# Kernel optimization log

Hardware: AMD Instinct MI355X
Metric: run time of the kernel (lower is better)

Reference implementation:

```python
import jax, jax.numpy as jnp
import numpy as np


def _conv3x3(x, W, b):
    # NCHW conv, stride 1, padding 1 (hard-coded in the torch module)
    y = jax.lax.conv_general_dilated(
        x, W, window_strides=(1, 1), padding=[(1, 1), (1, 1)],
        dimension_numbers=("NCHW", "OIHW", "NCHW"))
    return y + b[None, :, None, None]


def _grid_sample_bilinear(img, gx, gy):
    # img: [N,H,W]; gx,gy: [N,H,W] normalized coords in [-1,1].
    # Matches torch grid_sample(mode='bilinear', padding_mode='zeros',
    # align_corners=False).
    N, H, W = img.shape
    ix = ((gx + 1.0) * W - 1.0) * 0.5  # unnormalized x coord
    iy = ((gy + 1.0) * H - 1.0) * 0.5  # unnormalized y coord

    x0f = jnp.floor(ix)
    y0f = jnp.floor(iy)
    x0 = x0f.astype(jnp.int32)
    y0 = y0f.astype(jnp.int32)
    x1 = x0 + 1
    y1 = y0 + 1

    # bilinear weights
    wx1 = ix - x0f
    wy1 = iy - y0f
    wx0 = 1.0 - wx1
    wy0 = 1.0 - wy1

    n_idx = jnp.arange(N)[:, None, None]

    def gather(yi, xi):
        valid = (yi >= 0) & (yi < H) & (xi >= 0) & (xi < W)
        yc = jnp.clip(yi, 0, H - 1)
        xc = jnp.clip(xi, 0, W - 1)
        v = img[n_idx, yc, xc]
        return jnp.where(valid, v, 0.0)

    return (gather(y0, x0) * (wy0 * wx0)
            + gather(y0, x1) * (wy0 * wx1)
            + gather(y1, x0) * (wy1 * wx0)
            + gather(y1, x1) * (wy1 * wx1))


def setup_inputs() -> dict:
    key = jax.random.key(0)
    ks = jax.random.split(key, 7)
    B, Cin, Cout, H, W = 16, 64, 64, 128, 128
    fan_in = Cin * 3 * 3
    std = 1.0 / np.sqrt(fan_in)
    x = jax.random.normal(ks[0], (B, Cin, H, W), dtype=jnp.float32)
    Ws = jax.random.normal(ks[1], (Cout, Cin, 3, 3), dtype=jnp.float32) * std
    Wx = jax.random.normal(ks[2], (Cout, Cin, 3, 3), dtype=jnp.float32) * std
    Wy = jax.random.normal(ks[3], (Cout, Cin, 3, 3), dtype=jnp.float32) * std
    bs = jnp.zeros((Cout,), dtype=jnp.float32)
    bx = jnp.zeros((Cout,), dtype=jnp.float32)
    by = jnp.zeros((Cout,), dtype=jnp.float32)
    return {"x": x, "Ws": Ws, "bs": bs, "Wx": Wx, "bx": bx, "Wy": Wy, "by": by}


def reference(x, Ws, bs, Wx, bx, Wy, by):
    score = _conv3x3(x, Ws, bs)            # [B,C,H,W]
    gx = _conv3x3(x, Wx, bx)               # absolute grid x coords
    gy = _conv3x3(x, Wy, by)               # absolute grid y coords
    B, C, H, W = score.shape
    out = _grid_sample_bilinear(score.reshape(B * C, H, W),
                                gx.reshape(B * C, H, W),
                                gy.reshape(B * C, H, W))
    return out.reshape(B, C, H, W)
```

## Files before the change

kernel.cpp:

```cpp
#include <hip/hip_runtime.h>
#include <stdint.h>

typedef unsigned short ushort_t;
typedef short bf16x8 __attribute__((ext_vector_type(8)));
typedef float f32x4 __attribute__((ext_vector_type(4)));
typedef float f32x16 __attribute__((ext_vector_type(16)));
typedef unsigned int uint4v __attribute__((ext_vector_type(4)));

#define HW_ 16384

__device__ __forceinline__ float bf2f(ushort_t u){
  return __uint_as_float(((unsigned)u) << 16);
}
__device__ __forceinline__ ushort_t f2bf(float f){
  unsigned u = __float_as_uint(f);
  u += 0x7fffu + ((u >> 16) & 1u);
  return (ushort_t)(u >> 16);
}
#define MFMA __builtin_amdgcn_mfma_f32_32x32x16_bf16

__global__ __launch_bounds__(256) void k_repack(
    const float* __restrict__ Ws, const float* __restrict__ Wx,
    const float* __restrict__ Wy, ushort_t* __restrict__ Wp){
  int e = blockIdx.x*256 + threadIdx.x;
  if (e >= 6*36*64*8) return;
  int j = e & 7; int lane = (e >> 3) & 63; int tt = e >> 9;
  int ks = tt % 36; int mtg = tt / 36;
  int co = mtg*32 + (lane & 31);
  int tap = ks >> 2;
  int ci = (ks & 3)*16 + ((lane >> 5) & 1)*8 + j;
  const float* src; int c;
  if (co < 64)      { src = Ws; c = co;       }
  else if (co < 128){ src = Wx; c = co - 64;  }
  else              { src = Wy; c = co - 128; }
  float w = src[(c*64 + ci)*9 + tap];
  ushort_t hi = f2bf(w);
  if (mtg < 2){
    Wp[e] = hi;
  } else {
    int eg = e - 2*18432;
    Wp[36864  + eg] = hi;
    Wp[110592 + eg] = f2bf(w - bf2f(hi));
  }
}

__global__ __launch_bounds__(256, 2) void k_conv_all(
    const float* __restrict__ x, const ushort_t* __restrict__ Wp,
    const float* __restrict__ bs, const float* __restrict__ bx,
    const float* __restrict__ by,
    ushort_t* __restrict__ score, unsigned int* __restrict__ coords){
  int bid = blockIdx.x;
  int idx = bid >> 3;
  int b = (bid & 7) + 8*(idx >> 7);
  int rest = idx & 127;
  int h0 = (rest >> 1)*2;
  int wq = (rest & 1)*64;
  int t = threadIdx.x; int lane = t & 63; int wid = t >> 6;
  int n = lane & 31; int kh = lane >> 5;
  __shared__ __align__(16) ushort_t XL[2*16896];

  const float* xb = x + (size_t)b*64*HW_;
  #pragma unroll 3
  for (int it=0; it<9; it++){
    int f = it*256 + t;
    if (f < 2112){
      int r   = f / 528;
      int rem = f - r*528;
      int o   = rem / 66;
      int w1  = rem - o*66;
      int y = h0 + r - 1;
      int w = wq + w1 - 1;
      bf16x8 hv = {0,0,0,0,0,0,0,0}, lv = {0,0,0,0,0,0,0,0};
      if (((unsigned)y < 128u) & ((unsigned)w < 128u)){
        const float* p = xb + (size_t)(o*8)*HW_ + y*128 + w;
        #pragma unroll
        for (int j=0;j<8;j++){
          float fv = p[(size_t)j*HW_];
          ushort_t hi = f2bf(fv);
          hv[j] = (short)hi;
          lv[j] = (short)f2bf(fv - bf2f(hi));
        }
      }
      int addr = (r*66 + w1)*64 + ((o ^ (w1 & 7))<<3);
      *(bf16x8*)&XL[addr]         = hv;
      *(bf16x8*)&XL[16896 + addr] = lv;
    }
  }
  __syncthreads();

  int mh = wid & 1;
  int ph = wid >> 1;

  f32x16 acc_s[2], acc_x[2], acc_y[2];
  #pragma unroll
  for (int reg=0; reg<16; reg++){
    int col = mh*32 + (reg & 3) + 8*(reg >> 2) + 4*kh;
    float vs = bs[col], vx = bx[col], vy = by[col];
    #pragma unroll
    for (int ni=0; ni<2; ni++){
      acc_s[ni][reg] = vs; acc_x[ni][reg] = vx; acc_y[ni][reg] = vy;
    }
  }

  const ushort_t* aSb = Wp + mh*36*512 + lane*8;
  const ushort_t* aXh = Wp + 36864 + mh*36*512 + lane*8;
  const ushort_t* aYh = Wp + 36864 + (2+mh)*36*512 + lane*8;
  #pragma unroll
  for (int tap=0; tap<9; tap++){
    int rb = tap/3; int dw = tap - rb*3 - 1;
    int row = rb + ph;
    #pragma unroll
    for (int q=0; q<4; q++){
      int ks = tap*4 + q;
      bf16x8 s8 = *(const bf16x8*)&aSb[ks*512];
      bf16x8 xh = *(const bf16x8*)&aXh[ks*512];
      bf16x8 xl = *(const bf16x8*)&aXh[73728 + ks*512];
      bf16x8 yh = *(const bf16x8*)&aYh[ks*512];
      bf16x8 yl = *(const bf16x8*)&aYh[73728 + ks*512];
      #pragma unroll
      for (int ni=0; ni<2; ni++){
        int w1 = ni*32 + n + dw + 1;
        int off = (row*66 + w1)*64 + ((((q<<1)+kh) ^ (w1 & 7)) << 3);
        bf16x8 bh = *(const bf16x8*)&XL[off];
        bf16x8 bl = *(const bf16x8*)&XL[16896 + off];
        acc_s[ni] = MFMA(s8, bh, acc_s[ni], 0,0,0);
        acc_x[ni] = MFMA(xh, bh, acc_x[ni], 0,0,0);
        acc_y[ni] = MFMA(yh, bh, acc_y[ni], 0,0,0);
        acc_x[ni] = MFMA(xl, bh, acc_x[ni], 0,0,0);
        acc_y[ni] = MFMA(yl, bh, acc_y[ni], 0,0,0);
        acc_x[ni] = MFMA(xh, bl, acc_x[ni], 0,0,0);
        acc_y[ni] = MFMA(yh, bl, acc_y[ni], 0,0,0);
      }
    }
  }

  int h = h0 + ph;
  #pragma unroll
  for (int ni=0; ni<2; ni++){
    int w = wq + ni*32 + n;
    ushort_t*     sb = score  + (size_t)b*64*HW_ + h*128 + w;
    unsigned int* cb = coords + (size_t)b*64*HW_ + h*128 + w;
    #pragma unroll
    for (int reg=0; reg<16; reg++){
      int col = mh*32 + (reg & 3) + 8*(reg >> 2) + 4*kh;
      sb[(size_t)col*HW_] = f2bf(acc_s[ni][reg]);
      float ix = fminf(fmaxf((acc_x[ni][reg]+1.f)*64.f - 0.5f, -2.f), 129.f);
      float iy = fminf(fmaxf((acc_y[ni][reg]+1.f)*64.f - 0.5f, -2.f), 129.f);
      unsigned ux = (unsigned)rintf((ix+2.f)*480.f);
      unsigned uy = (unsigned)rintf((iy+2.f)*480.f);
      cb[(size_t)col*HW_] = ux | (uy << 16);
    }
  }
}

__global__ __launch_bounds__(256, 4) void k_sample(
    const ushort_t* __restrict__ score, const unsigned int* __restrict__ coords,
    float* __restrict__ out){
  int bid = blockIdx.x;
  int idx = bid >> 3;
  int b  = (bid & 7) + 8*(idx >> 6);
  int co = idx & 63;
  int t = threadIdx.x;
  __shared__ __align__(16) ushort_t SC[128*136];

  const ushort_t* sp = score + (size_t)(b*64 + co)*HW_;
  #pragma unroll
  for (int i=0;i<8;i++){
    int c = i*256 + t;
    int y = c >> 4; int xg = (c & 15)*8;
    *(bf16x8*)&SC[y*136 + xg] = *(const bf16x8*)(sp + c*8);
  }
  __syncthreads();

  const unsigned int* cp = coords + (size_t)(b*64 + co)*HW_;
  float* op = out + (size_t)(b*64 + co)*HW_;
  uint4v ca = *(const uint4v*)(cp + t*8);
  uint4v cb2 = *(const uint4v*)(cp + t*8 + 4);
  #pragma unroll 1
  for (int k=0;k<8;k++){
    int px = (k*256 + t)*8;
    uint4v na, nb;
    if (k < 7){
      na = *(const uint4v*)(cp + px + 2048);
      nb = *(const uint4v*)(cp + px + 2052);
    }
    float r[8];
    #pragma unroll
    for (int j=0;j<8;j++){
      unsigned u = (j < 4) ? ca[j] : cb2[j-4];
      float ix = (float)(u & 0xffffu)*(1.0f/480.0f) - 2.0f;
      float iy = (float)(u >> 16)   *(1.0f/480.0f) - 2.0f;
      float x0f = floorf(ix), y0f = floorf(iy);
      int x0 = (int)x0f, y0 = (int)y0f;
      float wx1 = ix - x0f, wy1 = iy - y0f;
      float wx0 = 1.f - wx1, wy0 = 1.f - wy1;
      int x0c = min(max(x0,0),127), x1c = min(max(x0+1,0),127);
      int y0c = min(max(y0,0),127), y1c = min(max(y0+1,0),127);
      bool vx0 = (unsigned)x0     < 128u, vx1 = (unsigned)(x0+1) < 128u;
      bool vy0 = (unsigned)y0     < 128u, vy1 = (unsigned)(y0+1) < 128u;
      float v00 = (vy0 && vx0) ? bf2f(SC[y0c*136 + x0c]) : 0.f;
      float v01 = (vy0 && vx1) ? bf2f(SC[y0c*136 + x1c]) : 0.f;
      float v10 = (vy1 && vx0) ? bf2f(SC[y1c*136 + x0c]) : 0.f;
      float v11 = (vy1 && vx1) ? bf2f(SC[y1c*136 + x1c]) : 0.f;
      r[j] = v00*(wy0*wx0) + v01*(wy0*wx1) + v10*(wy1*wx0) + v11*(wy1*wx1);
    }
    f32x4 r0 = {r[0],r[1],r[2],r[3]};
    f32x4 r1 = {r[4],r[5],r[6],r[7]};
    *(f32x4*)(op + px)     = r0;
    *(f32x4*)(op + px + 4) = r1;
    ca = na; cb2 = nb;
  }
}

extern "C" void kernel_launch(void* const* d_in, const int* in_sizes, int n_in,
                              void* d_out, int out_size, void* d_ws, size_t ws_size,
                              hipStream_t stream){
  const float* x  = (const float*)d_in[0];
  const float* Ws = (const float*)d_in[1];
  const float* bs = (const float*)d_in[2];
  const float* Wx = (const float*)d_in[3];
  const float* bx = (const float*)d_in[4];
  const float* Wy = (const float*)d_in[5];
  const float* by = (const float*)d_in[6];
  float* out = (float*)d_out;
  ushort_t* ws  = (ushort_t*)d_ws;
  ushort_t*     score  = ws;
  unsigned int* coords = (unsigned int*)(ws + 16777216);
  ushort_t*     Wp     = ws + 16777216 + 2*16777216;

  k_repack  <<<dim3(432),  256, 0, stream>>>(Ws, Wx, Wy, Wp);
  k_conv_all<<<dim3(2048), 256, 0, stream>>>(x, Wp, bs, bx, by, score, coords);
  k_sample  <<<dim3(1024), 256, 0, stream>>>(score, coords, out);
}
```

Baseline: 287.3 us.

## Switch conv to fp16 MFMA with int8 correction terms for coordinate convs

Replaces the bf16 hi/lo split convolution with fp16 MFMAs for the main products. The coordinate convolutions get their error-compensation cross terms from int8 MFMAs (32x32x32) on scaled residuals, so the compensation uses roughly half the number of high-precision MFMA issues. The shared-memory input tile is re-laid-out into one fp16 plane and two int8 planes, and weight repacking now produces fp16 plus int8 correction tiles. Score is stored as fp16 instead of bf16. This trades the bf16 split scheme for fixed-point scalings (x*16, residual*32768, w*512) that may lose accuracy for inputs outside the expected range.

Result: slower. 357.2 us (+24.3%).

```diff
diff --git a/kernel.cpp b/kernel.cpp
--- a/kernel.cpp
+++ b/kernel.cpp
@@ -2,50 +2,69 @@
 #include <stdint.h>
 
 typedef unsigned short ushort_t;
-typedef short bf16x8 __attribute__((ext_vector_type(8)));
+typedef _Float16 f16x8 __attribute__((ext_vector_type(8)));
 typedef float f32x4 __attribute__((ext_vector_type(4)));
 typedef float f32x16 __attribute__((ext_vector_type(16)));
+typedef int   i32x4 __attribute__((ext_vector_type(4)));
+typedef int   i32x16 __attribute__((ext_vector_type(16)));
 typedef unsigned int uint4v __attribute__((ext_vector_type(4)));
 
 #define HW_ 16384
-
-__device__ __forceinline__ float bf2f(ushort_t u){
-  return __uint_as_float(((unsigned)u) << 16);
-}
-__device__ __forceinline__ ushort_t f2bf(float f){
-  unsigned u = __float_as_uint(f);
-  u += 0x7fffu + ((u >> 16) & 1u);
-  return (ushort_t)(u >> 16);
-}
-#define MFMA __builtin_amdgcn_mfma_f32_32x32x16_bf16
+#define MFMAH  __builtin_amdgcn_mfma_f32_32x32x16_f16
+#define MFMAI8 __builtin_amdgcn_mfma_i32_32x32x32_i8
+#define C_CORR (1.0f/16777216.0f)
+
+__device__ __forceinline__ ushort_t f2h_bits(float f){
+  union { _Float16 h; ushort_t u; } c; c.h = (_Float16)f; return c.u;
+}
+__device__ __forceinline__ float h_bits2f(ushort_t u){
+  union { _Float16 h; ushort_t u; } c; c.u = u; return (float)c.h;
+}
+__device__ __forceinline__ int clamp8(int v){ return min(max(v,-127),127); }
 
 __global__ __launch_bounds__(256) void k_repack(
     const float* __restrict__ Ws, const float* __restrict__ Wx,
-    const float* __restrict__ Wy, ushort_t* __restrict__ Wp){
+    const float* __restrict__ Wy,
+    ushort_t* __restrict__ WpH, unsigned int* __restrict__ WpC){
   int e = blockIdx.x*256 + threadIdx.x;
-  if (e >= 6*36*64*8) return;
-  int j = e & 7; int lane = (e >> 3) & 63; int tt = e >> 9;
-  int ks = tt % 36; int mtg = tt / 36;
-  int co = mtg*32 + (lane & 31);
-  int tap = ks >> 2;
-  int ci = (ks & 3)*16 + ((lane >> 5) & 1)*8 + j;
-  const float* src; int c;
-  if (co < 64)      { src = Ws; c = co;       }
-  else if (co < 128){ src = Wx; c = co - 64;  }
-  else              { src = Wy; c = co - 128; }
-  float w = src[(c*64 + ci)*9 + tap];
-  ushort_t hi = f2bf(w);
-  if (mtg < 2){
-    Wp[e] = hi;
-  } else {
-    int eg = e - 2*18432;
-    Wp[36864  + eg] = hi;
-    Wp[110592 + eg] = f2bf(w - bf2f(hi));
+  if (e < 110592){
+    int j = e & 7; int lane = (e >> 3) & 63; int rest = e >> 9;
+    int ks = rest % 36; int cm = rest / 36;
+    int conv = cm >> 1; int mh = cm & 1;
+    int co = mh*32 + (lane & 31);
+    int tap = ks >> 2;
+    int ci = (ks & 3)*16 + ((lane >> 5) & 1)*8 + j;
+    const float* src = (conv==0) ? Ws : (conv==1) ? Wx : Wy;
+    WpH[e] = f2h_bits(src[(co*64 + ci)*9 + tap]);
+  } else if (e < 110592 + 36864){
+    int d = e - 110592;
+    int j4 = d & 3; int lane = (d >> 2) & 63; int rest = d >> 8;
+    int ks = rest % 18; int gm = rest / 18;
+    int g = gm >> 1; int mh = gm & 1;
+    int co = mh*32 + (lane & 31);
+    int tap = ks >> 1;
+    const float* src = (g==0 || g==2) ? Wx : Wy;
+    unsigned dd = 0;
+    #pragma unroll
+    for (int bb=0; bb<4; bb++){
+      int ci = (ks & 1)*32 + ((lane >> 5) & 1)*16 + j4*4 + bb;
+      float w = src[(co*64 + ci)*9 + tap];
+      int v;
+      if (g < 2){
+        v = clamp8((int)rintf(w*512.f));
+      } else {
+        float wl = w - h_bits2f(f2h_bits(w));
+        v = clamp8((int)rintf(wl*1048576.f));
+      }
+      dd |= ((unsigned)(v & 255)) << (bb*8);
+    }
+    WpC[d] = dd;
   }
 }
 
 __global__ __launch_bounds__(256, 2) void k_conv_all(
-    const float* __restrict__ x, const ushort_t* __restrict__ Wp,
+    const float* __restrict__ x,
+    const ushort_t* __restrict__ WpH, const unsigned int* __restrict__ WpC,
     const float* __restrict__ bs, const float* __restrict__ bx,
     const float* __restrict__ by,
     ushort_t* __restrict__ score, unsigned int* __restrict__ coords){
@@ -57,33 +76,42 @@
   int wq = (rest & 1)*64;
   int t = threadIdx.x; int lane = t & 63; int wid = t >> 6;
   int n = lane & 31; int kh = lane >> 5;
-  __shared__ __align__(16) ushort_t XL[2*16896];
+  __shared__ __align__(16) _Float16 BH[16896];
+  __shared__ __align__(16) char BAl[16896];
+  __shared__ __align__(16) char BAh[16896];
 
   const float* xb = x + (size_t)b*64*HW_;
-  #pragma unroll 3
-  for (int it=0; it<9; it++){
+  #pragma unroll
+  for (int it=0; it<5; it++){
     int f = it*256 + t;
-    if (f < 2112){
-      int r   = f / 528;
-      int rem = f - r*528;
-      int o   = rem / 66;
-      int w1  = rem - o*66;
-      int y = h0 + r - 1;
-      int w = wq + w1 - 1;
-      bf16x8 hv = {0,0,0,0,0,0,0,0}, lv = {0,0,0,0,0,0,0,0};
+    if (f < 1056){
+      int r = f/264; int rem = f - r*264; int q = rem/66; int w1 = rem - q*66;
+      int y = h0 + r - 1; int w = wq + w1 - 1;
+      f16x8 h0v = {0,0,0,0,0,0,0,0}, h1v = {0,0,0,0,0,0,0,0};
+      unsigned alb[4] = {0,0,0,0}, ahb[4] = {0,0,0,0};
       if (((unsigned)y < 128u) & ((unsigned)w < 128u)){
-        const float* p = xb + (size_t)(o*8)*HW_ + y*128 + w;
+        const float* p = xb + (size_t)(q*16)*HW_ + y*128 + w;
         #pragma unroll
-        for (int j=0;j<8;j++){
-          float fv = p[(size_t)j*HW_];
-          ushort_t hi = f2bf(fv);
-          hv[j] = (short)hi;
-          lv[j] = (short)f2bf(fv - bf2f(hi));
+        for (int j=0; j<16; j++){
+          float v = p[(size_t)j*HW_];
+          _Float16 hv = (_Float16)v;
+          float al = v - (float)hv;
+          int a8 = clamp8((int)rintf(al*32768.f));
+          int x8 = clamp8((int)rintf(v*16.f));
+          if (j < 8) h0v[j] = hv; else h1v[j-8] = hv;
+          alb[j>>2] |= ((unsigned)(a8 & 255)) << ((j&3)*8);
+          ahb[j>>2] |= ((unsigned)(x8 & 255)) << ((j&3)*8);
         }
       }
-      int addr = (r*66 + w1)*64 + ((o ^ (w1 & 7))<<3);
-      *(bf16x8*)&XL[addr]         = hv;
-      *(bf16x8*)&XL[16896 + addr] = lv;
+      int base = (r*66 + w1)*64;
+      int sw = w1 & 7;
+      *(f16x8*)&BH[base + (((2*q)   ^ sw) << 3)] = h0v;
+      *(f16x8*)&BH[base + (((2*q+1) ^ sw) << 3)] = h1v;
+      int islot = ((q + (w1 >> 1)) & 3) << 4;
+      i32x4 av = {(int)alb[0],(int)alb[1],(int)alb[2],(int)alb[3]};
+      i32x4 hv2 = {(int)ahb[0],(int)ahb[1],(int)ahb[2],(int)ahb[3]};
+      *(i32x4*)&BAl[base + islot] = av;
+      *(i32x4*)&BAh[base + islot] = hv2;
     }
   }
   __syncthreads();
@@ -91,45 +119,66 @@
   int mh = wid & 1;
   int ph = wid >> 1;
 
-  f32x16 acc_s[2], acc_x[2], acc_y[2];
-  #pragma unroll
-  for (int reg=0; reg<16; reg++){
-    int col = mh*32 + (reg & 3) + 8*(reg >> 2) + 4*kh;
-    float vs = bs[col], vx = bx[col], vy = by[col];
-    #pragma unroll
-    for (int ni=0; ni<2; ni++){
-      acc_s[ni][reg] = vs; acc_x[ni][reg] = vx; acc_y[ni][reg] = vy;
-    }
-  }
-
-  const ushort_t* aSb = Wp + mh*36*512 + lane*8;
-  const ushort_t* aXh = Wp + 36864 + mh*36*512 + lane*8;
-  const ushort_t* aYh = Wp + 36864 + (2+mh)*36*512 + lane*8;
+  f32x16 acc_s[2], gxh[2], gyh[2];
+  i32x16 cx[2], cy[2];
+  #pragma unroll
+  for (int ni=0; ni<2; ni++){
+    #pragma unroll
+    for (int r2=0; r2<16; r2++){
+      acc_s[ni][r2]=0.f; gxh[ni][r2]=0.f; gyh[ni][r2]=0.f;
+      cx[ni][r2]=0; cy[ni][r2]=0;
+    }
+  }
+
+  const ushort_t* aS = WpH + ((0*2+mh)*36)*512 + lane*8;
+  const ushort_t* aX = WpH + ((1*2+mh)*36)*512 + lane*8;
+  const ushort_t* aY = WpH + ((2*2+mh)*36)*512 + lane*8;
+  const char* cWhx = (const char*)WpC + (((0*2+mh)*18)*64 + lane)*16;
+  const char* cWhy = (const char*)WpC + (((1*2+mh)*18)*64 + lane)*16;
+  const char* cWlx = (const char*)WpC + (((2*2+mh)*18)*64 + lane)*16;
+  const char* cWly = (const char*)WpC + (((3*2+mh)*18)*64 + lane)*16;
+
   #pragma unroll
   for (int tap=0; tap<9; tap++){
     int rb = tap/3; int dw = tap - rb*3 - 1;
     int row = rb + ph;
     #pragma unroll
-    for (int q=0; q<4; q++){
-      int ks = tap*4 + q;
-      bf16x8 s8 = *(const bf16x8*)&aSb[ks*512];
-      bf16x8 xh = *(const bf16x8*)&aXh[ks*512];
-      bf16x8 xl = *(const bf16x8*)&aXh[73728 + ks*512];
-      bf16x8 yh = *(const bf16x8*)&aYh[ks*512];
-      bf16x8 yl = *(const bf16x8*)&aYh[73728 + ks*512];
+    for (int qp=0; qp<2; qp++){
+      int ksA = tap*4 + qp*2;
+      int ks32 = tap*2 + qp;
+      f16x8 sA = *(const f16x8*)&aS[ksA*512];
+      f16x8 sB = *(const f16x8*)&aS[(ksA+1)*512];
+      f16x8 xA = *(const f16x8*)&aX[ksA*512];
+      f16x8 xB = *(const f16x8*)&aX[(ksA+1)*512];
+      f16x8 yA = *(const f16x8*)&aY[ksA*512];
+      f16x8 yB = *(const f16x8*)&aY[(ksA+1)*512];
+      i32x4 whx = *(const i32x4*)&cWhx[ks32*1024];
+      i32x4 why = *(const i32x4*)&cWhy[ks32*1024];
+      i32x4 wlx = *(const i32x4*)&cWlx[ks32*1024];
+      i32x4 wly = *(const i32x4*)&cWly[ks32*1024];
+      int oA = qp*4 + kh;
+      int oB = qp*4 + 2 + kh;
+      int q2 = qp*2 + kh;
       #pragma unroll
       for (int ni=0; ni<2; ni++){
         int w1 = ni*32 + n + dw + 1;
-        int off = (row*66 + w1)*64 + ((((q<<1)+kh) ^ (w1 & 7)) << 3);
-        bf16x8 bh = *(const bf16x8*)&XL[off];
-        bf16x8 bl = *(const bf16x8*)&XL[16896 + off];
-        acc_s[ni] = MFMA(s8, bh, acc_s[ni], 0,0,0);
-        acc_x[ni] = MFMA(xh, bh, acc_x[ni], 0,0,0);
-        acc_y[ni] = MFMA(yh, bh, acc_y[ni], 0,0,0);
-        acc_x[ni] = MFMA(xl, bh, acc_x[ni], 0,0,0);
-        acc_y[ni] = MFMA(yl, bh, acc_y[ni], 0,0,0);
-        acc_x[ni] = MFMA(xh, bl, acc_x[ni], 0,0,0);
-        acc_y[ni] = MFMA(yh, bl, acc_y[ni], 0,0,0);
+        int rowb = (row*66 + w1)*64;
+        int sw = w1 & 7;
+        f16x8 bA = *(const f16x8*)&BH[rowb + ((oA ^ sw) << 3)];
+        f16x8 bB = *(const f16x8*)&BH[rowb + ((oB ^ sw) << 3)];
+        int islot = ((q2 + (w1 >> 1)) & 3) << 4;
+        i32x4 bal = *(const i32x4*)&BAl[rowb + islot];
+        i32x4 bah = *(const i32x4*)&BAh[rowb + islot];
+        acc_s[ni] = MFMAH(sA, bA, acc_s[ni], 0,0,0);
+        gxh[ni]   = MFMAH(xA, bA, gxh[ni],   0,0,0);
+        gyh[ni]   = MFMAH(yA, bA, gyh[ni],   0,0,0);
+        acc_s[ni] = MFMAH(sB, bB, acc_s[ni], 0,0,0);
+        gxh[ni]   = MFMAH(xB, bB, gxh[ni],   0,0,0);
+        gyh[ni]   = MFMAH(yB, bB, gyh[ni],   0,0,0);
+        cx[ni] = MFMAI8(whx, bal, cx[ni], 0,0,0);
+        cx[ni] = MFMAI8(wlx, bah, cx[ni], 0,0,0);
+        cy[ni] = MFMAI8(why, bal, cy[ni], 0,0,0);
+        cy[ni] = MFMAI8(wly, bah, cy[ni], 0,0,0);
       }
     }
   }
@@ -143,11 +192,14 @@
     #pragma unroll
     for (int reg=0; reg<16; reg++){
       int col = mh*32 + (reg & 3) + 8*(reg >> 2) + 4*kh;
-      sb[(size_t)col*HW_] = f2bf(acc_s[ni][reg]);
-      float ix = fminf(fmaxf((acc_x[ni][reg]+1.f)*64.f - 0.5f, -2.f), 129.f);
-      float iy = fminf(fmaxf((acc_y[ni][reg]+1.f)*64.f - 0.5f, -2.f), 129.f);
-      unsigned ux = (unsigned)rintf((ix+2.f)*480.f);
-      unsigned uy = (unsigned)rintf((iy+2.f)*480.f);
+      float sv = acc_s[ni][reg] + bs[col];
+      float gx = gxh[ni][reg] + (float)cx[ni][reg]*C_CORR + bx[col];
+      float gy = gyh[ni][reg] + (float)cy[ni][reg]*C_CORR + by[col];
+      sb[(size_t)col*HW_] = f2h_bits(sv);
+      float ix = fminf(fmaxf((gx + 1.f)*64.f - 0.5f, -2.f), 129.f);
+      float iy = fminf(fmaxf((gy + 1.f)*64.f - 0.5f, -2.f), 129.f);
+      unsigned ux = (unsigned)rintf((ix + 2.f)*480.f);
+      unsigned uy = (unsigned)rintf((iy + 2.f)*480.f);
       cb[(size_t)col*HW_] = ux | (uy << 16);
     }
   }
@@ -168,7 +220,7 @@
   for (int i=0;i<8;i++){
     int c = i*256 + t;
     int y = c >> 4; int xg = (c & 15)*8;
-    *(bf16x8*)&SC[y*136 + xg] = *(const bf16x8*)(sp + c*8);
+    *(f16x8*)&SC[y*136 + xg] = *(const f16x8*)(sp + c*8);
   }
   __syncthreads();
 
@@ -198,10 +250,10 @@
       int y0c = min(max(y0,0),127), y1c = min(max(y0+1,0),127);
       bool vx0 = (unsigned)x0     < 128u, vx1 = (unsigned)(x0+1) < 128u;
       bool vy0 = (unsigned)y0     < 128u, vy1 = (unsigned)(y0+1) < 128u;
-      float v00 = (vy0 && vx0) ? bf2f(SC[y0c*136 + x0c]) : 0.f;
-      float v01 = (vy0 && vx1) ? bf2f(SC[y0c*136 + x1c]) : 0.f;
-      float v10 = (vy1 && vx0) ? bf2f(SC[y1c*136 + x0c]) : 0.f;
-      float v11 = (vy1 && vx1) ? bf2f(SC[y1c*136 + x1c]) : 0.f;
+      float v00 = (vy0 && vx0) ? h_bits2f(SC[y0c*136 + x0c]) : 0.f;
+      float v01 = (vy0 && vx1) ? h_bits2f(SC[y0c*136 + x1c]) : 0.f;
+      float v10 = (vy1 && vx0) ? h_bits2f(SC[y1c*136 + x0c]) : 0.f;
+      float v11 = (vy1 && vx1) ? h_bits2f(SC[y1c*136 + x1c]) : 0.f;
       r[j] = v00*(wy0*wx0) + v01*(wy0*wx1) + v10*(wy1*wx0) + v11*(wy1*wx1);
     }
     f32x4 r0 = {r[0],r[1],r[2],r[3]};
@@ -226,9 +278,10 @@
   ushort_t* ws  = (ushort_t*)d_ws;
   ushort_t*     score  = ws;
   unsigned int* coords = (unsigned int*)(ws + 16777216);
-  ushort_t*     Wp     = ws + 16777216 + 2*16777216;
-
-  k_repack  <<<dim3(432),  256, 0, stream>>>(Ws, Wx, Wy, Wp);
-  k_conv_all<<<dim3(2048), 256, 0, stream>>>(x, Wp, bs, bx, by, score, coords);
+  ushort_t*     WpH    = ws + 50331648;
+  unsigned int* WpC    = (unsigned int*)(ws + 50331648 + 110592);
+
+  k_repack  <<<dim3(576),  256, 0, stream>>>(Ws, Wx, Wy, WpH, WpC);
+  k_conv_all<<<dim3(2048), 256, 0, stream>>>(x, WpH, WpC, bs, bx, by, score, coords);
   k_sample  <<<dim3(1024), 256, 0, stream>>>(score, coords, out);
 }
```
